# Kernel tuning notes

Hardware: AMD Instinct MI355X
Metric: run time of the kernel (lower is better)

## Reference

```python
import jax, jax.numpy as jnp
import numpy as np


def make_dictionary(T, Drr, Dtheta):
    # rows i=0..T-1; (-Drr)**i == (-1)**i * Drr**i for integer i
    idx = jnp.arange(T, dtype=Drr.dtype)[:, None]                      # [T,1]
    sign = jnp.where(jnp.arange(T)[:, None] % 2 == 0, 1.0, -1.0).astype(Drr.dtype)
    ri = Drr[None, :] ** idx                                           # [T,N]
    c = jnp.cos(idx * Dtheta[None, :])
    s = jnp.sin(idx * Dtheta[None, :])
    dic = jnp.concatenate(
        [jnp.ones((T, 1), Drr.dtype), ri * c, sign * ri * c, ri * s, sign * ri * s],
        axis=1,
    )                                                                  # [T, 1+4N]
    G = jnp.linalg.norm(dic, axis=0)
    G = jnp.where(G == 0, jnp.sqrt(jnp.asarray(T, dic.dtype)), G)
    return dic / G


def softshrink(x, lam):
    return jnp.sign(x) * jnp.maximum(jnp.abs(x) - lam, 0.0)


def fista(D, Y, lambd=0.1, max_iter=100, tol=1e-4):
    # D: [T,K], Y: [B,T,F]
    K = D.shape[1]
    DtD = D.T @ D                                                      # [K,K]
    linv = 1.0 / jnp.linalg.norm(DtD)  # torch.norm(DtD, 2) == Frobenius norm
    DtY = jnp.einsum('tk,btf->bkf', D, Y) * linv                       # [B,K,F]
    A = jnp.eye(K, dtype=D.dtype) - DtD * linv
    lam = lambd * linv
    x0 = jnp.zeros_like(DtY)

    def cond(s):
        _, _, _, it, done = s
        return (it < max_iter) & jnp.logical_not(done)

    def body(s):
        x_old, y_old, t, it, done = s
        x_new = softshrink(jnp.einsum('kj,bjf->bkf', A, y_old) + DtY, lam)
        t_new = (1.0 + jnp.sqrt(1.0 + 4.0 * t * t)) / 2.0
        tt = (t - 1.0) / t_new
        y_new = (1.0 + tt) * x_new - tt * x_old
        conv = jnp.linalg.norm((x_new - x_old).ravel()) / K < tol
        return (x_new, y_new, jnp.where(conv, t, t_new), it + 1, conv)

    s0 = (x0, x0, jnp.asarray(1.0, D.dtype), jnp.asarray(0, jnp.int32),
          jnp.asarray(False))
    x, _, _, _, _ = jax.lax.while_loop(cond, body, s0)
    return x


def setup_inputs() -> dict:
    key = jax.random.key(0)
    k1, k2, k3 = jax.random.split(key, 3)
    return {
        'x': jax.random.normal(k1, (2, 36, 20480), jnp.float32),
        'Drr': jax.random.uniform(k2, (40,), dtype=jnp.float32),
        'Dtheta': jax.random.uniform(k3, (40,), dtype=jnp.float32),
        'T': 36,
    }


def reference(x, Drr, Dtheta, T):
    D = make_dictionary(T, Drr, Dtheta)
    return fista(D, x, lambd=0.1, max_iter=100)
```

## Files before the change

### kernel.cpp

```cpp
#include <hip/hip_runtime.h>
#include <math.h>

typedef _Float16 half8 __attribute__((ext_vector_type(8)));
typedef _Float16 half4 __attribute__((ext_vector_type(4)));
typedef float    f32x4 __attribute__((ext_vector_type(4)));

#define T_DIM 36
#define N_AT 40
#define K_REAL 161
#define MT 11
#define KSM 5
#define KS2 2
#define B_DIM 2
#define F_DIM 20480
#define CB 16
#define NTHREADS 256
#define SETUP_T 512
#define MAXIT 100
#define YK 200
#define YST 72

#define WS_AFRAG_OFF 64
#define AFRAG_BYTES (MT * KSM * 2 * 1024)
#define WS_DFRAG_OFF (WS_AFRAG_OFF + AFRAG_BYTES)
#define DFRAG_BYTES (MT * KS2 * 2 * 1024)
#define WS_A160_OFF (WS_DFRAG_OFF + DFRAG_BYTES)

#define MFMA16(a, b, c) __builtin_amdgcn_mfma_f32_16x16x32_f16((a), (b), (c), 0, 0, 0)

__global__ void setup_kernel(const float* __restrict__ Drr,
                             const float* __restrict__ Dtheta,
                             float* __restrict__ ws) {
    __shared__ float Dl[K_REAL][T_DIM];
    __shared__ float red[SETUP_T];
    __shared__ float s_linv;
    int tid = threadIdx.x;

    if (tid < K_REAL) {
        float col[T_DIM];
        if (tid == 0) {
            for (int i = 0; i < T_DIM; ++i) col[i] = 1.0f;
        } else {
            int q = (tid - 1) / N_AT, n = (tid - 1) % N_AT;
            float r = Drr[n], th = Dtheta[n];
            float ri = 1.0f;
            for (int i = 0; i < T_DIM; ++i) {
                float c = cosf((float)i * th), s = sinf((float)i * th);
                float sign = (i & 1) ? -1.0f : 1.0f;
                float v;
                if (q == 0)      v = ri * c;
                else if (q == 1) v = sign * ri * c;
                else if (q == 2) v = ri * s;
                else             v = sign * ri * s;
                col[i] = v;
                ri *= r;
            }
        }
        float ss = 0.0f;
        for (int i = 0; i < T_DIM; ++i) ss += col[i] * col[i];
        float G = sqrtf(ss);
        float Ginv = (G == 0.0f) ? (1.0f / sqrtf((float)T_DIM)) : (1.0f / G);
        for (int i = 0; i < T_DIM; ++i) Dl[tid][i] = col[i] * Ginv;
    }
    __syncthreads();

    float local = 0.0f;
    for (int p = tid; p < K_REAL * K_REAL; p += SETUP_T) {
        int a = p / K_REAL, b = p % K_REAL;
        float dot = 0.0f;
        for (int i = 0; i < T_DIM; ++i) dot += Dl[a][i] * Dl[b][i];
        local += dot * dot;
    }
    red[tid] = local;
    __syncthreads();
    if (tid == 0) {
        float tot = 0.0f;
        for (int i = 0; i < SETUP_T; ++i) tot += red[i];
        float linv = 1.0f / sqrtf(tot);
        s_linv = linv;
        ws[0] = linv;
        ws[1] = 0.1f * linv;
    }
    __syncthreads();
    float linv = s_linv;

    _Float16* wsA = (_Float16*)((char*)ws + WS_AFRAG_OFF);
    int lane = tid >> 3, e = tid & 7;
    int fm = lane & 15, fq = lane >> 4;
    for (int p = 0; p < MT * KSM; ++p) {
        int Mt = p / KSM, ks = p % KSM;
        int m = Mt * 16 + fm;
        int k = ks * 32 + fq * 8 + e;
        float v = 0.0f;
        if (m < K_REAL) {
            float dot = 0.0f;
            for (int t = 0; t < T_DIM; ++t) dot += Dl[m][t] * Dl[k][t];
            v = ((m == k) ? 1.0f : 0.0f) - linv * dot;
        }
        _Float16 h = (_Float16)v;
        _Float16 l = (_Float16)(v - (float)h);
        int base = (p * 2) * 512 + lane * 8 + e;
        wsA[base]       = h;
        wsA[base + 512] = l;
    }

    _Float16* wsD = (_Float16*)((char*)ws + WS_DFRAG_OFF);
    for (int p = 0; p < MT * KS2; ++p) {
        int Mt = p / KS2, ks2 = p % KS2;
        int kr = Mt * 16 + fm;
        int t  = ks2 * 32 + fq * 8 + e;
        float v = (kr < K_REAL && t < T_DIM) ? linv * Dl[kr][t] : 0.0f;
        _Float16 h = (_Float16)v;
        _Float16 l = (_Float16)(v - (float)h);
        int base = (p * 2) * 512 + lane * 8 + e;
        wsD[base]       = h;
        wsD[base + 512] = l;
    }

    float* wsC = (float*)((char*)ws + WS_A160_OFF);
    if (tid < MT * 16) {
        int m = tid;
        float v = 0.0f;
        if (m < K_REAL) {
            float dot = 0.0f;
            for (int t = 0; t < T_DIM; ++t) dot += Dl[m][t] * Dl[160][t];
            v = ((m == 160) ? 1.0f : 0.0f) - linv * dot;
        }
        wsC[m] = v;
    }
}

__global__ void __launch_bounds__(NTHREADS, 2)
fista_mfma(const float* __restrict__ Y, const float* __restrict__ ws,
           float* __restrict__ out) {
    __shared__ __align__(16) _Float16 ybuf[2][2][CB][YK];

    const float lam = ((const float*)ws)[1];
    const half8* Afp = (const half8*)((const char*)ws + WS_AFRAG_OFF);
    const half8* Dfp = (const half8*)((const char*)ws + WS_DFRAG_OFF);
    const float* A160 = (const float*)((const char*)ws + WS_A160_OFF);

    const int tid  = threadIdx.x;
    const int lane = tid & 63;
    const int mg   = __builtin_amdgcn_readfirstlane(tid >> 6);
    const int mlc  = (mg == 3) ? 2 : 3;
    const int quad = lane >> 4;
    const int cl   = lane & 15;

    const int blk = blockIdx.x;
    const int b   = blk / (F_DIM / CB);
    const int f0  = (blk % (F_DIM / CB)) * CB;

    _Float16* Yst = &ybuf[1][0][0][0];
    const float* Yb = Y + (size_t)b * T_DIM * F_DIM + f0;
    for (int idx = tid; idx < 64 * CB; idx += NTHREADS) {
        int t = idx / CB, c = idx % CB;
        float v = (t < T_DIM) ? Yb[(size_t)t * F_DIM + c] : 0.0f;
        _Float16 h = (_Float16)v;
        _Float16 l = (_Float16)(v - (float)h);
        Yst[c * YST + t]            = h;
        Yst[CB * YST + c * YST + t] = l;
    }
    int4* zb = (int4*)&ybuf[0][0][0][0];
    for (int idx = tid; idx < (2 * CB * YK * 2) / 16; idx += NTHREADS)
        zb[idx] = int4{0, 0, 0, 0};
    __syncthreads();

    f32x4 dty[3];
    #pragma unroll
    for (int ml = 0; ml < 3; ++ml) dty[ml] = f32x4{0.f, 0.f, 0.f, 0.f};
    #pragma unroll
    for (int ks2 = 0; ks2 < KS2; ++ks2) {
        const _Float16* yp = Yst + cl * YST + ks2 * 32 + quad * 8;
        half8 yh = *(const half8*)yp;
        half8 yl = *(const half8*)(yp + CB * YST);
        #pragma unroll
        for (int ml = 0; ml < 3; ++ml) {
            if (ml < mlc) {
                int Mt = mg * 3 + ml;
                half8 dh = Dfp[((Mt * KS2 + ks2) * 2 + 0) * 64 + lane];
                half8 dl = Dfp[((Mt * KS2 + ks2) * 2 + 1) * 64 + lane];
                dty[ml] = MFMA16(dh, yh, dty[ml]);
                dty[ml] = MFMA16(dh, yl, dty[ml]);
                dty[ml] = MFMA16(dl, yh, dty[ml]);
            }
        }
    }
    __syncthreads();

    half8 Af[3][KSM][2];
    float a160[3][4];
    #pragma unroll
    for (int ml = 0; ml < 3; ++ml) {
        if (ml < mlc) {
            #pragma unroll
            for (int ks = 0; ks < KSM; ++ks)
                #pragma unroll
                for (int term = 0; term < 2; ++term)
                    Af[ml][ks][term] =
                        Afp[(((mg * 3 + ml) * KSM + ks) * 2 + term) * 64 + lane];
            #pragma unroll
            for (int r = 0; r < 4; ++r)
                a160[ml][r] = A160[(mg * 3 + ml) * 16 + quad * 4 + r];
        }
    }

    float xold[3][4];
    #pragma unroll
    for (int ml = 0; ml < 3; ++ml)
        #pragma unroll
        for (int r = 0; r < 4; ++r) xold[ml][r] = 0.0f;

    float tm = 1.0f;
    int p = 0;
    for (int it = 0; it < MAXIT; ++it) {
        f32x4 acc[3];
        #pragma unroll
        for (int ml = 0; ml < 3; ++ml) acc[ml] = dty[ml];

        {
            float y160 = (float)ybuf[p][0][cl][160] + (float)ybuf[p][1][cl][160];
            #pragma unroll
            for (int ml = 0; ml < 3; ++ml)
                if (ml < mlc)
                    #pragma unroll
                    for (int r = 0; r < 4; ++r)
                        acc[ml][r] += a160[ml][r] * y160;
        }

        #pragma unroll
        for (int ks = 0; ks < KSM; ++ks) {
            const _Float16* yp = &ybuf[p][0][cl][ks * 32 + quad * 8];
            half8 yh = *(const half8*)yp;
            half8 yl = *(const half8*)(yp + CB * YK);
            #pragma unroll
            for (int ml = 0; ml < 3; ++ml) {
                if (ml < mlc) {
                    acc[ml] = MFMA16(Af[ml][ks][0], yh, acc[ml]);
                    acc[ml] = MFMA16(Af[ml][ks][0], yl, acc[ml]);
                    acc[ml] = MFMA16(Af[ml][ks][1], yh, acc[ml]);
                }
            }
        }

        float tn = 0.5f * (1.0f + sqrtf(1.0f + 4.0f * tm * tm));
        float tt = (tm - 1.0f) / tn;
        tm = tn;

        #pragma unroll
        for (int ml = 0; ml < 3; ++ml) {
            if (ml < mlc) {
                half4 hv, lv;
                #pragma unroll
                for (int r = 0; r < 4; ++r) {
                    float v  = acc[ml][r];
                    float s  = fmaxf(fabsf(v) - lam, 0.0f);
                    float xn = copysignf(s, v);
                    float yn = (1.0f + tt) * xn - tt * xold[ml][r];
                    xold[ml][r] = xn;
                    _Float16 h = (_Float16)yn;
                    hv[r] = h;
                    lv[r] = (_Float16)(yn - (float)h);
                }
                int k0 = (mg * 3 + ml) * 16 + quad * 4;
                *(half4*)&ybuf[1 - p][0][cl][k0] = hv;
                *(half4*)&ybuf[1 - p][1][cl][k0] = lv;
            }
        }
        __syncthreads();
        p ^= 1;
    }

    float* ob = out + (size_t)b * K_REAL * F_DIM + f0 + cl;
    #pragma unroll
    for (int ml = 0; ml < 3; ++ml)
        if (ml < mlc)
            #pragma unroll
            for (int r = 0; r < 4; ++r) {
                int k = (mg * 3 + ml) * 16 + quad * 4 + r;
                if (k < K_REAL) ob[(size_t)k * F_DIM] = xold[ml][r];
            }
}

extern "C" void kernel_launch(void* const* d_in, const int* in_sizes, int n_in,
                              void* d_out, int out_size, void* d_ws, size_t ws_size,
                              hipStream_t stream) {
    const float* x      = (const float*)d_in[0];
    const float* Drr    = (const float*)d_in[1];
    const float* Dtheta = (const float*)d_in[2];
    float* out = (float*)d_out;
    float* ws  = (float*)d_ws;

    hipLaunchKernelGGL(setup_kernel, dim3(1), dim3(SETUP_T), 0, stream,
                       Drr, Dtheta, ws);
    hipLaunchKernelGGL(fista_mfma, dim3((B_DIM * F_DIM) / CB), dim3(NTHREADS),
                       0, stream, x, ws, out);
}
```

Before: 704.8 us.

## Process two 16-column groups per block to reuse A fragments across columns

```diff
diff --git a/kernel.cpp b/kernel.cpp
--- a/kernel.cpp
+++ b/kernel.cpp
@@ -13,7 +13,8 @@
 #define KS2 2
 #define B_DIM 2
 #define F_DIM 20480
-#define CB 16
+#define CB 32
+#define NG 2
 #define NTHREADS 256
 #define SETUP_T 512
 #define MAXIT 100
@@ -166,23 +167,28 @@
         zb[idx] = int4{0, 0, 0, 0};
     __syncthreads();
 
-    f32x4 dty[3];
-    #pragma unroll
-    for (int ml = 0; ml < 3; ++ml) dty[ml] = f32x4{0.f, 0.f, 0.f, 0.f};
+    f32x4 dty[3][NG];
+    #pragma unroll
+    for (int ml = 0; ml < 3; ++ml)
+        #pragma unroll
+        for (int ng = 0; ng < NG; ++ng) dty[ml][ng] = f32x4{0.f, 0.f, 0.f, 0.f};
     #pragma unroll
     for (int ks2 = 0; ks2 < KS2; ++ks2) {
-        const _Float16* yp = Yst + cl * YST + ks2 * 32 + quad * 8;
-        half8 yh = *(const half8*)yp;
-        half8 yl = *(const half8*)(yp + CB * YST);
-        #pragma unroll
-        for (int ml = 0; ml < 3; ++ml) {
-            if (ml < mlc) {
-                int Mt = mg * 3 + ml;
-                half8 dh = Dfp[((Mt * KS2 + ks2) * 2 + 0) * 64 + lane];
-                half8 dl = Dfp[((Mt * KS2 + ks2) * 2 + 1) * 64 + lane];
-                dty[ml] = MFMA16(dh, yh, dty[ml]);
-                dty[ml] = MFMA16(dh, yl, dty[ml]);
-                dty[ml] = MFMA16(dl, yh, dty[ml]);
+        #pragma unroll
+        for (int ng = 0; ng < NG; ++ng) {
+            const _Float16* yp = Yst + (ng * 16 + cl) * YST + ks2 * 32 + quad * 8;
+            half8 yh = *(const half8*)yp;
+            half8 yl = *(const half8*)(yp + CB * YST);
+            #pragma unroll
+            for (int ml = 0; ml < 3; ++ml) {
+                if (ml < mlc) {
+                    int Mt = mg * 3 + ml;
+                    half8 dh = Dfp[((Mt * KS2 + ks2) * 2 + 0) * 64 + lane];
+                    half8 dl = Dfp[((Mt * KS2 + ks2) * 2 + 1) * 64 + lane];
+                    dty[ml][ng] = MFMA16(dh, yh, dty[ml][ng]);
+                    dty[ml][ng] = MFMA16(dh, yl, dty[ml][ng]);
+                    dty[ml][ng] = MFMA16(dl, yh, dty[ml][ng]);
+                }
             }
         }
     }
@@ -205,40 +211,49 @@
         }
     }
 
-    float xold[3][4];
+    float xold[3][NG][4];
     #pragma unroll
     for (int ml = 0; ml < 3; ++ml)
         #pragma unroll
-        for (int r = 0; r < 4; ++r) xold[ml][r] = 0.0f;
+        for (int ng = 0; ng < NG; ++ng)
+            #pragma unroll
+            for (int r = 0; r < 4; ++r) xold[ml][ng][r] = 0.0f;
 
     float tm = 1.0f;
     int p = 0;
     for (int it = 0; it < MAXIT; ++it) {
-        f32x4 acc[3];
-        #pragma unroll
-        for (int ml = 0; ml < 3; ++ml) acc[ml] = dty[ml];
-
-        {
-            float y160 = (float)ybuf[p][0][cl][160] + (float)ybuf[p][1][cl][160];
+        f32x4 acc[3][NG];
+        #pragma unroll
+        for (int ml = 0; ml < 3; ++ml)
+            #pragma unroll
+            for (int ng = 0; ng < NG; ++ng) acc[ml][ng] = dty[ml][ng];
+
+        #pragma unroll
+        for (int ng = 0; ng < NG; ++ng) {
+            float y160 = (float)ybuf[p][0][ng * 16 + cl][160]
+                       + (float)ybuf[p][1][ng * 16 + cl][160];
             #pragma unroll
             for (int ml = 0; ml < 3; ++ml)
                 if (ml < mlc)
                     #pragma unroll
                     for (int r = 0; r < 4; ++r)
-                        acc[ml][r] += a160[ml][r] * y160;
+                        acc[ml][ng][r] += a160[ml][r] * y160;
         }
 
         #pragma unroll
         for (int ks = 0; ks < KSM; ++ks) {
-            const _Float16* yp = &ybuf[p][0][cl][ks * 32 + quad * 8];
-            half8 yh = *(const half8*)yp;
-            half8 yl = *(const half8*)(yp + CB * YK);
-            #pragma unroll
-            for (int ml = 0; ml < 3; ++ml) {
-                if (ml < mlc) {
-                    acc[ml] = MFMA16(Af[ml][ks][0], yh, acc[ml]);
-                    acc[ml] = MFMA16(Af[ml][ks][0], yl, acc[ml]);
-                    acc[ml] = MFMA16(Af[ml][ks][1], yh, acc[ml]);
+            #pragma unroll
+            for (int ng = 0; ng < NG; ++ng) {
+                const _Float16* yp = &ybuf[p][0][ng * 16 + cl][ks * 32 + quad * 8];
+                half8 yh = *(const half8*)yp;
+                half8 yl = *(const half8*)(yp + CB * YK);
+                #pragma unroll
+                for (int ml = 0; ml < 3; ++ml) {
+                    if (ml < mlc) {
+                        acc[ml][ng] = MFMA16(Af[ml][ks][0], yh, acc[ml][ng]);
+                        acc[ml][ng] = MFMA16(Af[ml][ks][0], yl, acc[ml][ng]);
+                        acc[ml][ng] = MFMA16(Af[ml][ks][1], yh, acc[ml][ng]);
+                    }
                 }
             }
         }
@@ -250,36 +265,42 @@
         #pragma unroll
         for (int ml = 0; ml < 3; ++ml) {
             if (ml < mlc) {
-                half4 hv, lv;
+                #pragma unroll
+                for (int ng = 0; ng < NG; ++ng) {
+                    half4 hv, lv;
+                    #pragma unroll
+                    for (int r = 0; r < 4; ++r) {
+                        float v  = acc[ml][ng][r];
+                        float s  = fmaxf(fabsf(v) - lam, 0.0f);
+                        float xn = copysignf(s, v);
+                        float yn = (1.0f + tt) * xn - tt * xold[ml][ng][r];
+                        xold[ml][ng][r] = xn;
+                        _Float16 h = (_Float16)yn;
+                        hv[r] = h;
+                        lv[r] = (_Float16)(yn - (float)h);
+                    }
+                    int k0 = (mg * 3 + ml) * 16 + quad * 4;
+                    *(half4*)&ybuf[1 - p][0][ng * 16 + cl][k0] = hv;
+                    *(half4*)&ybuf[1 - p][1][ng * 16 + cl][k0] = lv;
+                }
+            }
+        }
+        __syncthreads();
+        p ^= 1;
+    }
+
+    #pragma unroll
+    for (int ng = 0; ng < NG; ++ng) {
+        float* ob = out + (size_t)b * K_REAL * F_DIM + f0 + ng * 16 + cl;
+        #pragma unroll
+        for (int ml = 0; ml < 3; ++ml)
+            if (ml < mlc)
                 #pragma unroll
                 for (int r = 0; r < 4; ++r) {
-                    float v  = acc[ml][r];
-                    float s  = fmaxf(fabsf(v) - lam, 0.0f);
-                    float xn = copysignf(s, v);
-                    float yn = (1.0f + tt) * xn - tt * xold[ml][r];
-                    xold[ml][r] = xn;
-                    _Float16 h = (_Float16)yn;
-                    hv[r] = h;
-                    lv[r] = (_Float16)(yn - (float)h);
+                    int k = (mg * 3 + ml) * 16 + quad * 4 + r;
+                    if (k < K_REAL) ob[(size_t)k * F_DIM] = xold[ml][ng][r];
                 }
-                int k0 = (mg * 3 + ml) * 16 + quad * 4;
-                *(half4*)&ybuf[1 - p][0][cl][k0] = hv;
-                *(half4*)&ybuf[1 - p][1][cl][k0] = lv;
-            }
-        }
-        __syncthreads();
-        p ^= 1;
-    }
-
-    float* ob = out + (size_t)b * K_REAL * F_DIM + f0 + cl;
-    #pragma unroll
-    for (int ml = 0; ml < 3; ++ml)
-        if (ml < mlc)
-            #pragma unroll
-            for (int r = 0; r < 4; ++r) {
-                int k = (mg * 3 + ml) * 16 + quad * 4 + r;
-                if (k < K_REAL) ob[(size_t)k * F_DIM] = xold[ml][r];
-            }
+    }
 }
 
 extern "C" void kernel_launch(void* const* d_in, const int* in_sizes, int n_in,
```

Measured after the change: 682.5 us. 1.03x faster.

## Interleave two column groups per block to overlap MFMA sweep with epilogue

Applied to the files above, without the earlier changes.

```diff
diff --git a/kernel.cpp b/kernel.cpp
--- a/kernel.cpp
+++ b/kernel.cpp
@@ -13,7 +13,7 @@
 #define KS2 2
 #define B_DIM 2
 #define F_DIM 20480
-#define CB 16
+#define CB 32
 #define NTHREADS 256
 #define SETUP_T 512
 #define MAXIT 100
@@ -130,10 +130,68 @@
     }
 }
 
+template <int G>
+__device__ __forceinline__ void sweep_g(f32x4 (&acc)[3], const f32x4 (&dty)[3],
+                                        const half8 (&Af)[3][KSM][2],
+                                        const float (&a160)[3][4],
+                                        const _Float16 (*Yh)[YK],
+                                        const _Float16 (*Yl)[YK],
+                                        int cl, int quad, int mlc) {
+    #pragma unroll
+    for (int ks = 0; ks < KSM; ++ks) {
+        half8 yh = *(const half8*)&Yh[G * 16 + cl][ks * 32 + quad * 8];
+        half8 yl = *(const half8*)&Yl[G * 16 + cl][ks * 32 + quad * 8];
+        #pragma unroll
+        for (int ml = 0; ml < 3; ++ml) {
+            if (ml < mlc) {
+                f32x4 c0 = (ks == 0) ? dty[ml] : acc[ml];
+                c0 = MFMA16(Af[ml][ks][0], yh, c0);
+                c0 = MFMA16(Af[ml][ks][0], yl, c0);
+                acc[ml] = MFMA16(Af[ml][ks][1], yh, c0);
+            }
+        }
+    }
+    float y160 = (float)Yh[G * 16 + cl][160] + (float)Yl[G * 16 + cl][160];
+    #pragma unroll
+    for (int ml = 0; ml < 3; ++ml)
+        if (ml < mlc)
+            #pragma unroll
+            for (int r = 0; r < 4; ++r)
+                acc[ml][r] += a160[ml][r] * y160;
+}
+
+template <int G>
+__device__ __forceinline__ void epi_g(const f32x4 (&acc)[3], float (&xold)[3][4],
+                                      _Float16 (*Yh)[YK], _Float16 (*Yl)[YK],
+                                      float lam, float tt,
+                                      int cl, int quad, int mg, int mlc) {
+    #pragma unroll
+    for (int ml = 0; ml < 3; ++ml) {
+        if (ml < mlc) {
+            half4 hv, lv;
+            #pragma unroll
+            for (int r = 0; r < 4; ++r) {
+                float v  = acc[ml][r];
+                float s  = fmaxf(fabsf(v) - lam, 0.0f);
+                float xn = copysignf(s, v);
+                float yn = (1.0f + tt) * xn - tt * xold[ml][r];
+                xold[ml][r] = xn;
+                _Float16 h = (_Float16)yn;
+                hv[r] = h;
+                lv[r] = (_Float16)(yn - (float)h);
+            }
+            int k0 = (mg * 3 + ml) * 16 + quad * 4;
+            *(half4*)&Yh[G * 16 + cl][k0] = hv;
+            *(half4*)&Yl[G * 16 + cl][k0] = lv;
+        }
+    }
+}
+
 __global__ void __launch_bounds__(NTHREADS, 2)
 fista_mfma(const float* __restrict__ Y, const float* __restrict__ ws,
            float* __restrict__ out) {
-    __shared__ __align__(16) _Float16 ybuf[2][2][CB][YK];
+    __shared__ __align__(16) _Float16 Yh[CB][YK];
+    __shared__ __align__(16) _Float16 Yl[CB][YK];
 
     const float lam = ((const float*)ws)[1];
     const half8* Afp = (const half8*)((const char*)ws + WS_AFRAG_OFF);
@@ -151,42 +209,53 @@
     const int b   = blk / (F_DIM / CB);
     const int f0  = (blk % (F_DIM / CB)) * CB;
 
-    _Float16* Yst = &ybuf[1][0][0][0];
+    _Float16* sh = &Yh[0][0];
+    _Float16* sl = &Yl[0][0];
     const float* Yb = Y + (size_t)b * T_DIM * F_DIM + f0;
     for (int idx = tid; idx < 64 * CB; idx += NTHREADS) {
         int t = idx / CB, c = idx % CB;
         float v = (t < T_DIM) ? Yb[(size_t)t * F_DIM + c] : 0.0f;
         _Float16 h = (_Float16)v;
         _Float16 l = (_Float16)(v - (float)h);
-        Yst[c * YST + t]            = h;
-        Yst[CB * YST + c * YST + t] = l;
-    }
-    int4* zb = (int4*)&ybuf[0][0][0][0];
-    for (int idx = tid; idx < (2 * CB * YK * 2) / 16; idx += NTHREADS)
-        zb[idx] = int4{0, 0, 0, 0};
-    __syncthreads();
-
-    f32x4 dty[3];
-    #pragma unroll
-    for (int ml = 0; ml < 3; ++ml) dty[ml] = f32x4{0.f, 0.f, 0.f, 0.f};
+        sh[c * YST + t] = h;
+        sl[c * YST + t] = l;
+    }
+    __syncthreads();
+
+    f32x4 dty[2][3];
+    #pragma unroll
+    for (int g = 0; g < 2; ++g)
+        #pragma unroll
+        for (int ml = 0; ml < 3; ++ml) dty[g][ml] = f32x4{0.f, 0.f, 0.f, 0.f};
     #pragma unroll
     for (int ks2 = 0; ks2 < KS2; ++ks2) {
-        const _Float16* yp = Yst + cl * YST + ks2 * 32 + quad * 8;
-        half8 yh = *(const half8*)yp;
-        half8 yl = *(const half8*)(yp + CB * YST);
-        #pragma unroll
-        for (int ml = 0; ml < 3; ++ml) {
-            if (ml < mlc) {
-                int Mt = mg * 3 + ml;
-                half8 dh = Dfp[((Mt * KS2 + ks2) * 2 + 0) * 64 + lane];
-                half8 dl = Dfp[((Mt * KS2 + ks2) * 2 + 1) * 64 + lane];
-                dty[ml] = MFMA16(dh, yh, dty[ml]);
-                dty[ml] = MFMA16(dh, yl, dty[ml]);
-                dty[ml] = MFMA16(dl, yh, dty[ml]);
+        #pragma unroll
+        for (int g = 0; g < 2; ++g) {
+            half8 yh = *(const half8*)&sh[(g * 16 + cl) * YST + ks2 * 32 + quad * 8];
+            half8 yl = *(const half8*)&sl[(g * 16 + cl) * YST + ks2 * 32 + quad * 8];
+            #pragma unroll
+            for (int ml = 0; ml < 3; ++ml) {
+                if (ml < mlc) {
+                    int Mt = mg * 3 + ml;
+                    half8 dh = Dfp[((Mt * KS2 + ks2) * 2 + 0) * 64 + lane];
+                    half8 dl = Dfp[((Mt * KS2 + ks2) * 2 + 1) * 64 + lane];
+                    dty[g][ml] = MFMA16(dh, yh, dty[g][ml]);
+                    dty[g][ml] = MFMA16(dh, yl, dty[g][ml]);
+                    dty[g][ml] = MFMA16(dl, yh, dty[g][ml]);
+                }
             }
         }
     }
     __syncthreads();
+
+    {
+        int4* z1 = (int4*)&Yh[0][0];
+        int4* z2 = (int4*)&Yl[0][0];
+        for (int idx = tid; idx < (CB * YK * 2) / 16; idx += NTHREADS) {
+            z1[idx] = int4{0, 0, 0, 0};
+            z2[idx] = int4{0, 0, 0, 0};
+        }
+    }
 
     half8 Af[3][KSM][2];
     float a160[3][4];
@@ -204,82 +273,54 @@
                 a160[ml][r] = A160[(mg * 3 + ml) * 16 + quad * 4 + r];
         }
     }
-
-    float xold[3][4];
+    __syncthreads();
+
+    float xoldA[3][4], xoldB[3][4];
     #pragma unroll
     for (int ml = 0; ml < 3; ++ml)
         #pragma unroll
-        for (int r = 0; r < 4; ++r) xold[ml][r] = 0.0f;
-
-    float tm = 1.0f;
-    int p = 0;
-    for (int it = 0; it < MAXIT; ++it) {
-        f32x4 acc[3];
-        #pragma unroll
-        for (int ml = 0; ml < 3; ++ml) acc[ml] = dty[ml];
-
-        {
-            float y160 = (float)ybuf[p][0][cl][160] + (float)ybuf[p][1][cl][160];
-            #pragma unroll
-            for (int ml = 0; ml < 3; ++ml)
-                if (ml < mlc)
-                    #pragma unroll
-                    for (int r = 0; r < 4; ++r)
-                        acc[ml][r] += a160[ml][r] * y160;
-        }
-
-        #pragma unroll
-        for (int ks = 0; ks < KSM; ++ks) {
-            const _Float16* yp = &ybuf[p][0][cl][ks * 32 + quad * 8];
-            half8 yh = *(const half8*)yp;
-            half8 yl = *(const half8*)(yp + CB * YK);
-            #pragma unroll
-            for (int ml = 0; ml < 3; ++ml) {
-                if (ml < mlc) {
-                    acc[ml] = MFMA16(Af[ml][ks][0], yh, acc[ml]);
-                    acc[ml] = MFMA16(Af[ml][ks][0], yl, acc[ml]);
-                    acc[ml] = MFMA16(Af[ml][ks][1], yh, acc[ml]);
-                }
-            }
-        }
-
+        for (int r = 0; r < 4; ++r) { xoldA[ml][r] = 0.0f; xoldB[ml][r] = 0.0f; }
+
+    f32x4 accA[3], accB[3];
+    #pragma unroll
+    for (int ml = 0; ml < 3; ++ml) { accA[ml] = dty[0][ml]; accB[ml] = dty[1][ml]; }
+
+    float tm = 1.61803398875f;
+    float tt_prev = 0.0f;
+
+    epi_g<0>(accA, xoldA, Yh, Yl, lam, tt_prev, cl, quad, mg, mlc);
+    __syncthreads();
+
+    for (int s = 2; s <= MAXIT; ++s) {
         float tn = 0.5f * (1.0f + sqrtf(1.0f + 4.0f * tm * tm));
-        float tt = (tm - 1.0f) / tn;
+        float tt_cur = (tm - 1.0f) / tn;
         tm = tn;
 
-        #pragma unroll
-        for (int ml = 0; ml < 3; ++ml) {
-            if (ml < mlc) {
-                half4 hv, lv;
+        sweep_g<0>(accA, dty[0], Af, a160, Yh, Yl, cl, quad, mlc);
+        epi_g<1>(accB, xoldB, Yh, Yl, lam, tt_prev, cl, quad, mg, mlc);
+        __syncthreads();
+
+        sweep_g<1>(accB, dty[1], Af, a160, Yh, Yl, cl, quad, mlc);
+        epi_g<0>(accA, xoldA, Yh, Yl, lam, tt_cur, cl, quad, mg, mlc);
+        __syncthreads();
+
+        tt_prev = tt_cur;
+    }
+    epi_g<1>(accB, xoldB, Yh, Yl, lam, tt_prev, cl, quad, mg, mlc);
+
+    #pragma unroll
+    for (int g = 0; g < 2; ++g) {
+        float* ob = out + (size_t)b * K_REAL * F_DIM + f0 + g * 16 + cl;
+        #pragma unroll
+        for (int ml = 0; ml < 3; ++ml)
+            if (ml < mlc)
                 #pragma unroll
                 for (int r = 0; r < 4; ++r) {
-                    float v  = acc[ml][r];
-                    float s  = fmaxf(fabsf(v) - lam, 0.0f);
-                    float xn = copysignf(s, v);
-                    float yn = (1.0f + tt) * xn - tt * xold[ml][r];
-                    xold[ml][r] = xn;
-                    _Float16 h = (_Float16)yn;
-                    hv[r] = h;
-                    lv[r] = (_Float16)(yn - (float)h);
+                    int k = (mg * 3 + ml) * 16 + quad * 4 + r;
+                    float xv = g ? xoldB[ml][r] : xoldA[ml][r];
+                    if (k < K_REAL) ob[(size_t)k * F_DIM] = xv;
                 }
-                int k0 = (mg * 3 + ml) * 16 + quad * 4;
-                *(half4*)&ybuf[1 - p][0][cl][k0] = hv;
-                *(half4*)&ybuf[1 - p][1][cl][k0] = lv;
-            }
-        }
-        __syncthreads();
-        p ^= 1;
-    }
-
-    float* ob = out + (size_t)b * K_REAL * F_DIM + f0 + cl;
-    #pragma unroll
-    for (int ml = 0; ml < 3; ++ml)
-        if (ml < mlc)
-            #pragma unroll
-            for (int r = 0; r < 4; ++r) {
-                int k = (mg * 3 + ml) * 16 + quad * 4 + r;
-                if (k < K_REAL) ob[(size_t)k * F_DIM] = xold[ml][r];
-            }
+    }
 }
 
 extern "C" void kernel_launch(void* const* d_in, const int* in_sizes, int n_in,
```

New measurement: 678.5 us. 1.04x faster.
